# Performance work log

Measured on AMD Instinct MI355X. Metric: run time of the kernel, lower is better.

Reference implementation:

```python
import jax, jax.numpy as jnp
import numpy as np

TEMPERATURE = 8.0  # sqrt(d_k=64)
NEG_FILL = -1000.0


def setup_inputs() -> dict:
    key = jax.random.key(0)
    k1, k2, k3, k4 = jax.random.split(key, 4)
    B, Lq, Lk, D = 16, 2048, 2048, 64
    q = jax.random.normal(k1, (B, Lq, D), dtype=jnp.float32)
    k = jax.random.normal(k2, (B, Lk, D), dtype=jnp.float32)
    v = jax.random.normal(k3, (B, Lk, D), dtype=jnp.float32)
    pad_mask = jax.random.randint(k4, (B, Lk), 0, 2).astype(bool)
    return {"q": q, "k": k, "v": v, "pad_mask": pad_mask}


def reference(q, k, v, pad_mask):
    # scores: [B, Lq, Lk]
    attn = jnp.einsum('bqd,bkd->bqk', q, k) / TEMPERATURE
    # mask padded keys (broadcast over query dim, like pad_mask.unsqueeze(1))
    attn = jnp.where(pad_mask[:, None, :], NEG_FILL, attn)
    attn = jax.nn.softmax(attn, axis=-1)
    # dropout is identity in eval / p=0
    output = jnp.einsum('bqk,bkd->bqd', attn, v)
    return output, attn
```

## Files before the change

kernel.cpp:

```cpp
#include <hip/hip_runtime.h>
#include <hip/hip_bf16.h>

#define BB 16
#define LL 2048
#define DD 64

typedef __attribute__((ext_vector_type(8))) short short8t;
typedef __attribute__((ext_vector_type(4))) float f32x4;
typedef __attribute__((ext_vector_type(4))) unsigned short ushort4t;

__device__ __forceinline__ unsigned short f2bf(float x) {
  union { float f; unsigned int u; } c; c.f = x;
  unsigned int u = c.u;
  u += 0x7fffu + ((u >> 16) & 1u);
  return (unsigned short)(u >> 16);
}

__global__ void cvt_bf16(const float* __restrict__ in, unsigned short* __restrict__ out) {
  int i = (blockIdx.x * 256 + threadIdx.x) * 4;
  float4 v = *(const float4*)(in + i);
  ushort4t o;
  o.x = f2bf(v.x); o.y = f2bf(v.y); o.z = f2bf(v.z); o.w = f2bf(v.w);
  *(ushort4t*)(out + i) = o;
}

__global__ void vtrans(const float* __restrict__ v, unsigned short* __restrict__ vt) {
  __shared__ unsigned short t[64][66];
  int b = blockIdx.x >> 5, j0 = (blockIdx.x & 31) * 64;
  const float* src = v + ((size_t)b * LL + j0) * DD;
#pragma unroll
  for (int i = 0; i < 16; ++i) {
    int lin = i * 256 + threadIdx.x;
    int j = lin >> 6, d = lin & 63;
    t[j][d] = f2bf(src[lin]);
  }
  __syncthreads();
  unsigned short* dst = vt + (size_t)b * DD * LL;
#pragma unroll
  for (int i = 0; i < 16; ++i) {
    int lin = i * 256 + threadIdx.x;
    int d = lin >> 6, j = lin & 63;
    dst[(size_t)d * LL + j0 + j] = t[j][d];
  }
}

__device__ __forceinline__ void async_cp16(const unsigned short* src, unsigned short* dst_lds) {
  __builtin_amdgcn_global_load_lds(
      (const __attribute__((address_space(1))) unsigned int*)src,
      (__attribute__((address_space(3))) unsigned int*)dst_lds, 16, 0, 0);
}

__global__ void __launch_bounds__(256, 2)
attn_main(const unsigned short* __restrict__ Qb, const unsigned short* __restrict__ Kb,
          const unsigned short* __restrict__ VTb, const int* __restrict__ mask,
          float* __restrict__ out, float* __restrict__ attn) {
  __shared__ __align__(16) unsigned short TB[4][10240];
  float* redF = (float*)&TB[0][8192];
  float* rinvF = redF + 256;

  const int tid = threadIdx.x;
  const int w = tid >> 6;
  const int l = tid & 63;
  const int l15 = l & 15;
  const int g = l >> 4;

  const int swz = (blockIdx.x & 7) * 64 + (blockIdx.x >> 3);
  const int b = swz >> 5;
  const int q0 = (swz & 31) << 6;

  unsigned short* K0 = &TB[w][0];
  unsigned short* K1 = &TB[w][2048];
  unsigned short* V0 = &TB[w][4096];
  unsigned short* V1 = &TB[w][6144];
  unsigned short* PB = &TB[w][8192];

  const unsigned short* Kbb = Kb + (size_t)b * LL * DD;
  const unsigned short* VTbb = VTb + (size_t)b * DD * LL;
  const int* maskb = mask + b * LL;

  auto loadK = [&](int k0, unsigned short* KB) {
    const unsigned short* gs = Kbb + (size_t)k0 * DD;
#pragma unroll
    for (int i2 = 0; i2 < 4; ++i2) {
      int row = i2 * 8 + (l >> 3);
      int ce = (l & 7) * 8;
      async_cp16(gs + row * 64 + (ce ^ ((row & 3) << 4)), KB + i2 * 512);
    }
  };
  auto loadV = [&](int k0, unsigned short* VB) {
    const unsigned short* gs = VTbb + k0;
#pragma unroll
    for (int i2 = 0; i2 < 4; ++i2) {
      int row = i2 * 16 + (l >> 2);
      int ce = (l & 3) * 8;
      async_cp16(gs + (size_t)row * LL + (ce ^ ((row & 1) << 4)), VB + i2 * 512);
    }
  };

  short8t qf[4][2];
  {
    const unsigned short* qbase = Qb + ((size_t)b * LL + q0 + l15) * DD + 8 * g;
#pragma unroll
    for (int mi = 0; mi < 4; ++mi)
#pragma unroll
      for (int h = 0; h < 2; ++h)
        qf[mi][h] = *(const short8t*)(qbase + mi * 16 * DD + 32 * h);
  }

  float ls[4][4];
#pragma unroll
  for (int mi = 0; mi < 4; ++mi)
#pragma unroll
    for (int r = 0; r < 4; ++r) ls[mi][r] = 0.f;

  auto stepA = [&](int t, int tn, unsigned short* KBc, unsigned short* KBn,
                   int mk0c, int mk1c, int& mk0n, int& mk1n) {
    asm volatile("s_waitcnt vmcnt(0)" ::: "memory");
    loadK(tn * 32, KBn);
    mk0n = maskb[tn * 32 + l15];
    mk1n = maskb[tn * 32 + 16 + l15];

    short8t kf[2][2];
#pragma unroll
    for (int ni = 0; ni < 2; ++ni)
#pragma unroll
      for (int h = 0; h < 2; ++h) {
        int row = 16 * ni + l15;
        int col = (32 * h + 8 * g) ^ ((l15 & 3) << 4);
        kf[ni][h] = *(const short8t*)(KBc + row * 64 + col);
      }

    f32x4 sacc[4][2] = {};
    __builtin_amdgcn_s_setprio(1);
#pragma unroll
    for (int mi = 0; mi < 4; ++mi)
#pragma unroll
      for (int ni = 0; ni < 2; ++ni)
#pragma unroll
        for (int h = 0; h < 2; ++h)
          sacc[mi][ni] = __builtin_amdgcn_mfma_f32_16x16x32_bf16(qf[mi][h], kf[ni][h], sacc[mi][ni], 0, 0, 0);
    __builtin_amdgcn_s_setprio(0);
#pragma unroll
    for (int mi = 0; mi < 4; ++mi)
#pragma unroll
      for (int ni = 0; ni < 2; ++ni) {
        int mk = ni ? mk1c : mk0c;
#pragma unroll
        for (int r = 0; r < 4; ++r) {
          float p = mk ? 0.f : __expf(sacc[mi][ni][r] * 0.125f);
          ls[mi][r] += p;
        }
      }
  };

  {
    loadK(w * 32, K0);
    int a0 = maskb[w * 32 + l15], a1 = maskb[w * 32 + 16 + l15];
    int b0, b1;
    for (int j = 0; j < 8; ++j) {
      int t = w + 8 * j;
      stepA(t, t + 4, K0, K1, a0, a1, b0, b1);
      int t2 = t + 4;
      int tn = (j == 7) ? w : (t2 + 4);
      stepA(t2, tn, K1, K0, b0, b1, a0, a1);
    }
  }

#pragma unroll
  for (int mi = 0; mi < 4; ++mi)
#pragma unroll
    for (int r = 0; r < 4; ++r) {
      float s = ls[mi][r];
      s += __shfl_xor(s, 1);
      s += __shfl_xor(s, 2);
      s += __shfl_xor(s, 4);
      s += __shfl_xor(s, 8);
      if (l15 == 0) redF[w * 64 + 16 * mi + 4 * g + r] = s;
    }
  __syncthreads();
  if (tid < 64)
    rinvF[tid] = 1.0f / (redF[tid] + redF[64 + tid] + redF[128 + tid] + redF[192 + tid]);
  __syncthreads();

  float rinv_[4][4];
#pragma unroll
  for (int mi = 0; mi < 4; ++mi)
#pragma unroll
    for (int r = 0; r < 4; ++r) rinv_[mi][r] = rinvF[16 * mi + 4 * g + r];
  __syncthreads();

  f32x4 oacc[4][4] = {};
  auto stepB = [&](int t, int tn, const unsigned short* KBc, unsigned short* KBn,
                   const unsigned short* VBc, unsigned short* VBn,
                   int mk0c, int mk1c, int& mk0n, int& mk1n) {
    asm volatile("s_waitcnt vmcnt(32)" ::: "memory");
    const int k0 = t * 32;

    loadK(tn * 32, KBn);
    loadV(tn * 32, VBn);
    mk0n = maskb[tn * 32 + l15];
    mk1n = maskb[tn * 32 + 16 + l15];

    short8t kf[2][2], vf[4];
#pragma unroll
    for (int ni = 0; ni < 2; ++ni)
#pragma unroll
      for (int h = 0; h < 2; ++h) {
        int row = 16 * ni + l15;
        int col = (32 * h + 8 * g) ^ ((l15 & 3) << 4);
        kf[ni][h] = *(const short8t*)(KBc + row * 64 + col);
      }
#pragma unroll
    for (int ni = 0; ni < 4; ++ni)
      vf[ni] = *(const short8t*)(VBc + (16 * ni + l15) * 32 + ((8 * g) ^ ((l & 1) << 4)));

    f32x4 sacc[4][2] = {};
    __builtin_amdgcn_s_setprio(1);
#pragma unroll
    for (int mi = 0; mi < 4; ++mi)
#pragma unroll
      for (int ni = 0; ni < 2; ++ni)
#pragma unroll
        for (int h = 0; h < 2; ++h)
          sacc[mi][ni] = __builtin_amdgcn_mfma_f32_16x16x32_bf16(qf[mi][h], kf[ni][h], sacc[mi][ni], 0, 0, 0);
    __builtin_amdgcn_s_setprio(0);

#pragma unroll
    for (int mi = 0; mi < 4; ++mi)
#pragma unroll
      for (int ni = 0; ni < 2; ++ni) {
        int mk = ni ? mk1c : mk0c;
#pragma unroll
        for (int r = 0; r < 4; ++r) {
          float p = mk ? 0.f : __expf(sacc[mi][ni][r] * 0.125f) * rinv_[mi][r];
          int qloc = 16 * mi + 4 * g + r;
          attn[((size_t)(b * LL + q0 + qloc)) * LL + k0 + 16 * ni + l15] = p;
          PB[qloc * 32 + ((16 * ni + l15) ^ ((r & 1) << 4))] = f2bf(p);
        }
      }

    short8t pf[4];
#pragma unroll
    for (int mi = 0; mi < 4; ++mi)
      pf[mi] = *(const short8t*)(PB + (16 * mi + l15) * 32 + ((8 * g) ^ ((l & 1) << 4)));
    __builtin_amdgcn_s_setprio(1);
#pragma unroll
    for (int mi = 0; mi < 4; ++mi)
#pragma unroll
      for (int ni = 0; ni < 4; ++ni)
        oacc[mi][ni] = __builtin_amdgcn_mfma_f32_16x16x32_bf16(pf[mi], vf[ni], oacc[mi][ni], 0, 0, 0);
    __builtin_amdgcn_s_setprio(0);
  };

  {
    loadK(w * 32, K0);
    loadV(w * 32, V0);
    int a0 = maskb[w * 32 + l15], a1 = maskb[w * 32 + 16 + l15];
    asm volatile("s_waitcnt vmcnt(0)" ::: "memory");
    int b0, b1;
    for (int j = 0; j < 8; ++j) {
      int t = w + 8 * j;
      stepB(t, t + 4, K0, K1, V0, V1, a0, a1, b0, b1);
      int t2 = t + 4;
      int tn = (j == 7) ? w : (t2 + 4);
      stepB(t2, tn, K1, K0, V1, V0, b0, b1, a0, a1);
    }
  }

  asm volatile("s_waitcnt vmcnt(0)" ::: "memory");

  __syncthreads();
  float* OB = (float*)&TB[0][0];
  if (w) {
#pragma unroll
    for (int mi = 0; mi < 4; ++mi)
#pragma unroll
      for (int ni = 0; ni < 4; ++ni)
#pragma unroll
        for (int r = 0; r < 4; ++r)
          OB[(w - 1) * 4096 + (16 * mi + 4 * g + r) * 64 + 16 * ni + l15] = oacc[mi][ni][r];
  }
  __syncthreads();
  if (w == 0) {
#pragma unroll
    for (int mi = 0; mi < 4; ++mi)
#pragma unroll
      for (int ni = 0; ni < 4; ++ni)
#pragma unroll
        for (int r = 0; r < 4; ++r) {
          int pos = (16 * mi + 4 * g + r) * 64 + 16 * ni + l15;
          float o = oacc[mi][ni][r] + OB[pos] + OB[4096 + pos] + OB[8192 + pos];
          out[((size_t)(b * LL + q0 + 16 * mi + 4 * g + r)) * DD + 16 * ni + l15] = o;
        }
  }
}

extern "C" void kernel_launch(void* const* d_in, const int* in_sizes, int n_in,
                              void* d_out, int out_size, void* d_ws, size_t ws_size,
                              hipStream_t stream) {
  const float* q = (const float*)d_in[0];
  const float* k = (const float*)d_in[1];
  const float* v = (const float*)d_in[2];
  const int* pm = (const int*)d_in[3];

  float* out = (float*)d_out;
  float* attn = out + (size_t)BB * LL * DD;

  unsigned short* Qb = (unsigned short*)d_ws;
  unsigned short* Kb = Qb + (size_t)BB * LL * DD;
  unsigned short* VT = Kb + (size_t)BB * LL * DD;

  cvt_bf16<<<2048, 256, 0, stream>>>(q, Qb);
  cvt_bf16<<<2048, 256, 0, stream>>>(k, Kb);
  vtrans<<<512, 256, 0, stream>>>(v, VT);
  attn_main<<<512, 256, 0, stream>>>(Qb, Kb, VT, pm, out, attn);
}
```

Measured before the change: 94.71 us.

## Stage attention probabilities in LDS for coalesced float4 stores and single-buffer V

Softmax probabilities are now written as fp32 to a per-wave LDS tile, then read back so that the attn matrix is stored to global memory as contiguous float4 rows. Previously each lane wrote scalar floats with a 16-lane-wide pattern. The same fp32 tile is converted to bf16 when loading the P fragments for the PV MFMA. The V tile drops from double to single buffering. Next-tile K/V/mask loads are now issued only after the current LDS fragments are read, and the wait counts are adjusted to match. The final output reduction is also staged in LDS so it can be written with float4 stores. The aim is better write coalescing on the large attn output, at the cost of extra LDS traffic and less prefetch depth for V.

```diff
diff --git a/kernel.cpp b/kernel.cpp
--- a/kernel.cpp
+++ b/kernel.cpp
@@ -55,7 +55,7 @@
           const unsigned short* __restrict__ VTb, const int* __restrict__ mask,
           float* __restrict__ out, float* __restrict__ attn) {
   __shared__ __align__(16) unsigned short TB[4][10240];
-  float* redF = (float*)&TB[0][8192];
+  float* redF = (float*)&TB[0][6144];
   float* rinvF = redF + 256;
 
   const int tid = threadIdx.x;
@@ -64,15 +64,14 @@
   const int l15 = l & 15;
   const int g = l >> 4;
 
-  const int swz = (blockIdx.x & 7) * 64 + (blockIdx.x >> 3);
-  const int b = swz >> 5;
-  const int q0 = (swz & 31) << 6;
+  const int swzb = (blockIdx.x & 7) * 64 + (blockIdx.x >> 3);
+  const int b = swzb >> 5;
+  const int q0 = (swzb & 31) << 6;
 
   unsigned short* K0 = &TB[w][0];
   unsigned short* K1 = &TB[w][2048];
-  unsigned short* V0 = &TB[w][4096];
-  unsigned short* V1 = &TB[w][6144];
-  unsigned short* PB = &TB[w][8192];
+  unsigned short* VB = &TB[w][4096];
+  float* PF = (float*)&TB[w][6144];
 
   const unsigned short* Kbb = Kb + (size_t)b * LL * DD;
   const unsigned short* VTbb = VTb + (size_t)b * DD * LL;
@@ -87,7 +86,7 @@
       async_cp16(gs + row * 64 + (ce ^ ((row & 3) << 4)), KB + i2 * 512);
     }
   };
-  auto loadV = [&](int k0, unsigned short* VB) {
+  auto loadV = [&](int k0) {
     const unsigned short* gs = VTbb + k0;
 #pragma unroll
     for (int i2 = 0; i2 < 4; ++i2) {
@@ -190,16 +189,11 @@
   __syncthreads();
 
   f32x4 oacc[4][4] = {};
+  const size_t arow = (size_t)b * LL + q0;
   auto stepB = [&](int t, int tn, const unsigned short* KBc, unsigned short* KBn,
-                   const unsigned short* VBc, unsigned short* VBn,
                    int mk0c, int mk1c, int& mk0n, int& mk1n) {
-    asm volatile("s_waitcnt vmcnt(32)" ::: "memory");
+    asm volatile("s_waitcnt vmcnt(8)" ::: "memory");
     const int k0 = t * 32;
-
-    loadK(tn * 32, KBn);
-    loadV(tn * 32, VBn);
-    mk0n = maskb[tn * 32 + l15];
-    mk1n = maskb[tn * 32 + 16 + l15];
 
     short8t kf[2][2], vf[4];
 #pragma unroll
@@ -212,7 +206,14 @@
       }
 #pragma unroll
     for (int ni = 0; ni < 4; ++ni)
-      vf[ni] = *(const short8t*)(VBc + (16 * ni + l15) * 32 + ((8 * g) ^ ((l & 1) << 4)));
+      vf[ni] = *(const short8t*)(VB + (16 * ni + l15) * 32 + ((8 * g) ^ ((l & 1) << 4)));
+    asm volatile("s_waitcnt lgkmcnt(0)" ::: "memory");
+    __builtin_amdgcn_sched_barrier(0);
+
+    loadK(tn * 32, KBn);
+    mk0n = maskb[tn * 32 + l15];
+    mk1n = maskb[tn * 32 + 16 + l15];
+    loadV(tn * 32);
 
     f32x4 sacc[4][2] = {};
     __builtin_amdgcn_s_setprio(1);
@@ -233,16 +234,32 @@
 #pragma unroll
         for (int r = 0; r < 4; ++r) {
           float p = mk ? 0.f : __expf(sacc[mi][ni][r] * 0.125f) * rinv_[mi][r];
-          int qloc = 16 * mi + 4 * g + r;
-          attn[((size_t)(b * LL + q0 + qloc)) * LL + k0 + 16 * ni + l15] = p;
-          PB[qloc * 32 + ((16 * ni + l15) ^ ((r & 1) << 4))] = f2bf(p);
+          PF[(16 * mi + 4 * g + r) * 32 + ((16 * ni + l15) ^ ((g & 1) << 4))] = p;
         }
       }
 
+#pragma unroll
+    for (int it = 0; it < 8; ++it) {
+      int row = it * 8 + (l >> 3);
+      int c4 = (l & 7) * 4;
+      float4 pv = *(const float4*)(PF + row * 32 + (c4 ^ (((row >> 2) & 1) << 4)));
+      *(float4*)(attn + (arow + row) * LL + k0 + c4) = pv;
+    }
+
     short8t pf[4];
 #pragma unroll
-    for (int mi = 0; mi < 4; ++mi)
-      pf[mi] = *(const short8t*)(PB + (16 * mi + l15) * 32 + ((8 * g) ^ ((l & 1) << 4)));
+    for (int mi = 0; mi < 4; ++mi) {
+      int qq = 16 * mi + l15;
+      const float* src = PF + qq * 32 + ((8 * g) ^ (((l15 >> 2) & 1) << 4));
+      float4 pa = *(const float4*)(src);
+      float4 pb = *(const float4*)(src + 4);
+      short8t f;
+      f[0] = (short)f2bf(pa.x); f[1] = (short)f2bf(pa.y);
+      f[2] = (short)f2bf(pa.z); f[3] = (short)f2bf(pa.w);
+      f[4] = (short)f2bf(pb.x); f[5] = (short)f2bf(pb.y);
+      f[6] = (short)f2bf(pb.z); f[7] = (short)f2bf(pb.w);
+      pf[mi] = f;
+    }
     __builtin_amdgcn_s_setprio(1);
 #pragma unroll
     for (int mi = 0; mi < 4; ++mi)
@@ -254,16 +271,16 @@
 
   {
     loadK(w * 32, K0);
-    loadV(w * 32, V0);
     int a0 = maskb[w * 32 + l15], a1 = maskb[w * 32 + 16 + l15];
+    loadV(w * 32);
     asm volatile("s_waitcnt vmcnt(0)" ::: "memory");
     int b0, b1;
     for (int j = 0; j < 8; ++j) {
       int t = w + 8 * j;
-      stepB(t, t + 4, K0, K1, V0, V1, a0, a1, b0, b1);
+      stepB(t, t + 4, K0, K1, a0, a1, b0, b1);
       int t2 = t + 4;
       int tn = (j == 7) ? w : (t2 + 4);
-      stepB(t2, tn, K1, K0, V1, V0, b0, b1, a0, a1);
+      stepB(t2, tn, K1, K0, b0, b1, a0, a1);
     }
   }
 
@@ -289,9 +306,17 @@
 #pragma unroll
         for (int r = 0; r < 4; ++r) {
           int pos = (16 * mi + 4 * g + r) * 64 + 16 * ni + l15;
-          float o = oacc[mi][ni][r] + OB[pos] + OB[4096 + pos] + OB[8192 + pos];
-          out[((size_t)(b * LL + q0 + 16 * mi + 4 * g + r)) * DD + 16 * ni + l15] = o;
+          OB[12288 + pos] = oacc[mi][ni][r] + OB[pos] + OB[4096 + pos] + OB[8192 + pos];
         }
+  }
+  __syncthreads();
+#pragma unroll
+  for (int it = 0; it < 4; ++it) {
+    int lin = it * 256 + tid;
+    int row = lin >> 4;
+    int c4 = (lin & 15) * 4;
+    float4 o4 = *(const float4*)(OB + 12288 + row * 64 + c4);
+    *(float4*)(out + ((size_t)(b * LL + q0 + row)) * DD + c4) = o4;
   }
 }
 
```

Result: faster. 90.50 us (-4.5%).
